# Kernel optimization log

Hardware: AMD Instinct MI355X
Metric: run time of the kernel (lower is better)

Reference implementation:

```python
import jax, jax.numpy as jnp
import numpy as np

N = 50000      # nodes
E = 800000     # edges (before self loops)
IN = 128       # in_channels
HID = 128      # 2*out_channels
OUT = 64       # out_channels
NEG_SLOPE = 0.2


def _gat_conv(x, src, dst, W, a_src, a_dst, b, n_nodes):
    """Single-head PyG GATConv (concat=True, heads=1, self-loops already added)."""
    h = x @ W                                   # [N, F]
    alpha_s = h @ a_src                         # [N]
    alpha_d = h @ a_dst                         # [N]
    e = alpha_s[src] + alpha_d[dst]             # [E'] logits per edge j->i
    e = jnp.where(e > 0, e, NEG_SLOPE * e)      # LeakyReLU(0.2)
    # segment softmax over destination node
    m = jax.ops.segment_max(e, dst, num_segments=n_nodes)   # [N]
    w = jnp.exp(e - m[dst])                                   # [E']
    denom = jax.ops.segment_sum(w, dst, num_segments=n_nodes) # [N]
    alpha = w / denom[dst]                                     # [E']
    out = jax.ops.segment_sum(alpha[:, None] * h[src], dst, num_segments=n_nodes)
    return out + b


def _with_self_loops(edge_index, n_nodes):
    loop = jnp.arange(n_nodes, dtype=edge_index.dtype)
    src = jnp.concatenate([edge_index[0], loop])
    dst = jnp.concatenate([edge_index[1], loop])
    return src, dst


def setup_inputs() -> dict:
    key = jax.random.key(0)
    ks = jax.random.split(key, 10)
    s = 0.1
    return {
        "x": jax.random.normal(ks[0], (N, IN), jnp.float32),
        "edge_index": jax.random.randint(ks[1], (2, E), 0, N, jnp.int32),
        "W1": jax.random.normal(ks[2], (IN, HID), jnp.float32) * s,
        "a1_src": jax.random.normal(ks[3], (HID,), jnp.float32) * s,
        "a1_dst": jax.random.normal(ks[4], (HID,), jnp.float32) * s,
        "b1": jnp.zeros((HID,), jnp.float32),
        "W2": jax.random.normal(ks[5], (HID, OUT), jnp.float32) * s,
        "a2_src": jax.random.normal(ks[6], (OUT,), jnp.float32) * s,
        "a2_dst": jax.random.normal(ks[7], (OUT,), jnp.float32) * s,
        "b2": jnp.zeros((OUT,), jnp.float32),
    }


def reference(x, edge_index, W1, a1_src, a1_dst, b1, W2, a2_src, a2_dst, b2):
    src, dst = _with_self_loops(edge_index, N)
    h = _gat_conv(x, src, dst, W1, a1_src, a1_dst, b1, N)
    h = jax.nn.relu(h)
    return _gat_conv(h, src, dst, W2, a2_src, a2_dst, b2, N)
```

## Files before the change

### kernel.cpp

```cpp
#include <hip/hip_runtime.h>
#include <hip/hip_bf16.h>


#define BCAP 4096

typedef __attribute__((ext_vector_type(8))) short bf16x8;
typedef __attribute__((ext_vector_type(4))) float f32x4;
typedef __attribute__((ext_vector_type(2))) float f32x2;

__device__ __forceinline__ unsigned short bf16bits(float f){
  __hip_bfloat16 b = __float2bfloat16(f);
  return *(unsigned short*)&b;
}
__device__ __forceinline__ float bf16lo(unsigned int v){ return __uint_as_float(v << 16); }
__device__ __forceinline__ float bf16hi(unsigned int v){ return __uint_as_float(v & 0xFFFF0000u); }
__device__ __forceinline__ f32x2 up2(unsigned int u){
  f32x2 r; r.x = __uint_as_float(u << 16); r.y = __uint_as_float(u & 0xFFFF0000u);
  return r;
}
__device__ __forceinline__ float leaky_exp(float e){
  e = (e > 0.f) ? e : 0.2f*e;
  return __expf(e);
}

__global__ __launch_bounds__(256) void prep_all(
    const float* __restrict__ W1, const float* __restrict__ W2,
    const float* __restrict__ a2s, const float* __restrict__ a2d,
    unsigned short* __restrict__ W1t, unsigned short* __restrict__ W2t,
    float* __restrict__ vas, float* __restrict__ vad,
    int* __restrict__ bucketCount)
{
  int b = blockIdx.x, t = threadIdx.x;
  if (b < 48){
    int idx = b*256 + t;
    if (idx < 8192){
      int n = idx >> 6, k2 = idx & 63;
      float a = W1[(size_t)(2*k2)*128 + n];
      float c = W1[(size_t)(2*k2+1)*128 + n];
      ushort2 o; o.x = bf16bits(a); o.y = bf16bits(c);
      *(ushort2*)&W1t[(size_t)n*128 + 2*k2] = o;
    } else {
      int r = idx - 8192;
      int n = r >> 6, k2 = r & 63;
      float a = W2[(size_t)(2*k2)*64 + n];
      float c = W2[(size_t)(2*k2+1)*64 + n];
      ushort2 o; o.x = bf16bits(a); o.y = bf16bits(c);
      *(ushort2*)&W2t[(size_t)n*128 + 2*k2] = o;
    }
  } else if (b == 48){
    int k = t & 127;
    const float* av = (t < 128) ? a2s : a2d;
    float* ov = (t < 128) ? vas : vad;
    float s = 0.f;
    for (int n=0; n<64; n++) s += W2[(size_t)k*64 + n] * av[n];
    ov[k] = s;
  } else {
    bucketCount[t] = 0; bucketCount[t+256] = 0;
  }
}

template<int NC, bool FUSE>
__device__ __forceinline__ void gemm_body(
    const float* __restrict__ Af, const unsigned short* __restrict__ Ah,
    const unsigned short* __restrict__ Wt,
    const float* __restrict__ avs, const float* __restrict__ avd,
    unsigned short* __restrict__ H, float* __restrict__ as_, float* __restrict__ ad_,
    int M, int rowBase, unsigned short* As, unsigned short* Ws)
{
  const int K = 128;
  int t = threadIdx.x;
  if (Af){
    #pragma unroll
    for (int i=0;i<8;i++){
      int idx = t + i*256; int r = idx>>5, k4 = idx&31;
      int grow = rowBase + r;
      float4 v = (grow<M) ? *(const float4*)&Af[(size_t)grow*K + k4*4]
                          : make_float4(0.f,0.f,0.f,0.f);
      ushort4 o; o.x=bf16bits(v.x); o.y=bf16bits(v.y); o.z=bf16bits(v.z); o.w=bf16bits(v.w);
      *(ushort4*)&As[r*136 + k4*4] = o;
    }
  } else {
    #pragma unroll
    for (int i=0;i<4;i++){
      int idx = t + i*256; int r = idx>>4, k8 = idx&15;
      int grow = rowBase + r;
      uint4 v = (grow<M) ? *(const uint4*)&Ah[(size_t)grow*K + k8*8]
                         : make_uint4(0u,0u,0u,0u);
      *(uint4*)&As[r*136 + k8*8] = v;
    }
  }
  int wave = t>>6, lane = t&63, ln = lane&15, q = lane>>4;
  f32x4 acc[NC/16];
  #pragma unroll
  for (int nt=0; nt<NC/16; nt++) acc[nt] = (f32x4){0.f,0.f,0.f,0.f};

  #pragma unroll
  for (int ch=0; ch<NC/64; ++ch){
    __syncthreads();
    #pragma unroll
    for (int i=0;i<4;i++){
      int idx = t + i*256; int n = idx>>4, k8 = idx&15;
      *(uint4*)&Ws[n*136 + k8*8] = *(const uint4*)&Wt[(size_t)(ch*64+n)*K + k8*8];
    }
    __syncthreads();
    #pragma unroll
    for (int kk=0;kk<4;kk++){
      bf16x8 a = *(const bf16x8*)&As[(wave*16+ln)*136 + kk*32 + q*8];
      #pragma unroll
      for (int nt=0; nt<4; nt++){
        bf16x8 b = *(const bf16x8*)&Ws[(nt*16+ln)*136 + kk*32 + q*8];
        acc[ch*4+nt] = __builtin_amdgcn_mfma_f32_16x16x32_bf16(a, b, acc[ch*4+nt], 0, 0, 0);
      }
    }
  }
  float asl[NC/16], adl[NC/16];
  if (FUSE){
    #pragma unroll
    for (int nt=0; nt<NC/16; nt++){ asl[nt]=avs[nt*16+ln]; adl[nt]=avd[nt*16+ln]; }
  }
  #pragma unroll
  for (int i=0;i<4;i++){
    int grow = rowBase + wave*16 + q*4 + i;
    if (grow < M){
      float ps=0.f, pd=0.f;
      #pragma unroll
      for (int nt=0; nt<NC/16; nt++){
        float v = acc[nt][i];
        H[(size_t)grow*NC + nt*16 + ln] = bf16bits(v);
        if (FUSE){ ps += v*asl[nt]; pd += v*adl[nt]; }
      }
      if (FUSE){
        #pragma unroll
        for (int d=1; d<16; d<<=1){ ps += __shfl_xor(ps,d); pd += __shfl_xor(pd,d); }
        if (ln==0){ as_[grow] = ps; ad_[grow] = pd; }
      }
    }
  }
}

__global__ __launch_bounds__(256) void scatter_or_gemm(
    const int* __restrict__ src, const int* __restrict__ dst,
    int* __restrict__ bucketCount, unsigned int* __restrict__ gbuf, int E, int SB,
    const float* __restrict__ x, const unsigned short* __restrict__ W1t,
    const float* __restrict__ a1s, const float* __restrict__ a1d,
    unsigned short* __restrict__ h1, float* __restrict__ as1, float* __restrict__ ad1,
    int M)
{
  __shared__ unsigned short smem[64*136 + 64*136];
  int t = threadIdx.x;
  if ((int)blockIdx.x >= SB){
    gemm_body<128, true>(x, nullptr, W1t, a1s, a1d, h1, as1, ad1, M,
                         (blockIdx.x - SB)*64, smem, smem + 64*136);
    return;
  }
  int* hist = (int*)smem;
  int* base = hist + 512;
  int e0 = blockIdx.x * 4096;
  hist[t] = 0; hist[t+256] = 0;
  __syncthreads();
  int sv[16], dv[16];
  #pragma unroll
  for (int k=0;k<16;k++){
    int i = e0 + t + k*256;
    if (i < E){ sv[k]=src[i]; dv[k]=dst[i]; atomicAdd(&hist[dv[k]>>7], 1); }
    else { sv[k] = -1; dv[k] = 0; }
  }
  __syncthreads();
  int h0 = hist[t], h1c = hist[t+256];
  if (h0 > 0)  base[t]     = atomicAdd(&bucketCount[t],     h0);
  if (h1c > 0) base[t+256] = atomicAdd(&bucketCount[t+256], h1c);
  __syncthreads();
  hist[t] = 0; hist[t+256] = 0;
  __syncthreads();
  #pragma unroll
  for (int k=0;k<16;k++){
    if (sv[k] >= 0){
      int b = dv[k] >> 7;
      int r = base[b] + atomicAdd(&hist[b], 1);
      if (r < BCAP)
        gbuf[(size_t)b*BCAP + r] = ((unsigned)(dv[k] & 127) << 16) | (unsigned)sv[k];
    }
  }
}

__global__ __launch_bounds__(512) void fine_sort(
    const unsigned int* __restrict__ gbuf, const int* __restrict__ bucketCount,
    int* __restrict__ offs, int* __restrict__ srcS,
    const float* __restrict__ as1, const float* __restrict__ ad1,
    float* __restrict__ wS1, unsigned short* __restrict__ dstS,
    int N, int E, int B)
{
  __shared__ int sh[512];
  __shared__ int h[128];
  __shared__ int pre[128];
  __shared__ int rank[128];
  int b = blockIdx.x, t = threadIdx.x;
  {
    int nd_t = 0;
    if (t < B){ int lo=t*128; nd_t = (N-lo<128)?(N-lo):128; }
    sh[t] = (t < B ? bucketCount[t] : 0) + nd_t;
    __syncthreads();
    for (int d=1; d<512; d<<=1){
      int x = (t >= d) ? sh[t-d] : 0;
      __syncthreads();
      sh[t] += x;
      __syncthreads();
    }
  }
  int cnt = bucketCount[b]; if (cnt > BCAP) cnt = BCAP;
  int lo = b*128;
  int nd = (N - lo < 128) ? (N - lo) : 128;
  int base = sh[b] - (cnt + nd);
  if (b == 0 && t == 0) offs[N] = E + N;
  if (t < 128){ h[t] = 0; rank[t] = 0; }
  __syncthreads();
  for (int i = t; i < cnt; i += 512)
    atomicAdd(&h[(gbuf[(size_t)b*BCAP + i] >> 16) & 127], 1);
  __syncthreads();
  if (t < 128) pre[t] = (t < nd) ? (h[t] + 1) : 0;
  __syncthreads();
  for (int d=1; d<128; d<<=1){
    int x = (t >= d && t < 128) ? pre[t-d] : 0;
    __syncthreads();
    if (t < 128) pre[t] += x;
    __syncthreads();
  }
  int seg = (t < nd) ? (h[t] + 1) : 0;
  int ex  = (t < 128) ? (pre[t] - seg) : 0;
  if (t < nd){
    int v = lo + t;
    offs[v] = base + ex;
    srcS[base + ex] = v;
    wS1[base + ex]  = leaky_exp(as1[v] + ad1[v]);
    dstS[base + ex] = (unsigned short)v;
  }
  __syncthreads();
  if (t < 128) pre[t] = ex;
  __syncthreads();
  for (int i = t; i < cnt; i += 512){
    unsigned e = gbuf[(size_t)b*BCAP + i];
    int dl = (e >> 16) & 127;
    int s  = e & 0xFFFF;
    int r  = atomicAdd(&rank[dl], 1);
    int pos = base + pre[dl] + 1 + r;
    srcS[pos] = s;
    wS1[pos]  = leaky_exp(as1[s] + ad1[lo + dl]);
    dstS[pos] = (unsigned short)(lo + dl);
  }
}

__global__ __launch_bounds__(256) void edge_agg128(
    const int* __restrict__ offs, const int* __restrict__ srcS,
    const float* __restrict__ wS,
    const unsigned short* __restrict__ Hin, const float* __restrict__ bias,
    unsigned short* __restrict__ outp,
    const float* __restrict__ vas, const float* __restrict__ vad,
    float* __restrict__ as2, float* __restrict__ ad2, int n)
{
  int wid  = (blockIdx.x * 256 + threadIdx.x) >> 6;
  int lane = threadIdx.x & 63;
  int qw = lane >> 4, ql = lane & 15;
  int v = wid*4 + qw;
  bool alive = (v < n);
  int beg = 0, end = 0;
  if (alive){ beg = offs[v]; end = offs[v+1]; }
  f32x2 acc2[4];
  #pragma unroll
  for (int c=0;c<4;c++) acc2[c] = (f32x2){0.f, 0.f};
  float dn = 0.f;
  for (int base = beg; base < end; base += 16){
    int m = end - base; if (m > 16) m = 16;
    int sv = 0; float wv = 0.f;
    if (ql < m){ sv = srcS[base + ql]; wv = wS[base + ql]; }
    for (int j = 0; j < m; j += 4){
      int l0 = (qw<<4) + j;
      int   s0 = __shfl(sv,l0),   s1 = __shfl(sv,l0+1);
      int   s2 = __shfl(sv,l0+2), s3 = __shfl(sv,l0+3);
      float w0 = __shfl(wv,l0),   w1 = __shfl(wv,l0+1);
      float w2 = __shfl(wv,l0+2), w3 = __shfl(wv,l0+3);
      uint4 ha = *(const uint4*)&Hin[(size_t)s0*128 + ql*8];
      uint4 hb = *(const uint4*)&Hin[(size_t)s1*128 + ql*8];
      uint4 hc = *(const uint4*)&Hin[(size_t)s2*128 + ql*8];
      uint4 hd = *(const uint4*)&Hin[(size_t)s3*128 + ql*8];
      dn += (w0 + w1) + (w2 + w3);
      acc2[0] += w0*up2(ha.x) + w1*up2(hb.x) + w2*up2(hc.x) + w3*up2(hd.x);
      acc2[1] += w0*up2(ha.y) + w1*up2(hb.y) + w2*up2(hc.y) + w3*up2(hd.y);
      acc2[2] += w0*up2(ha.z) + w1*up2(hb.z) + w2*up2(hc.z) + w3*up2(hd.z);
      acc2[3] += w0*up2(ha.w) + w1*up2(hb.w) + w2*up2(hc.w) + w3*up2(hd.w);
    }
  }
  if (alive){
    float accf[8];
    #pragma unroll
    for (int c=0;c<4;c++){ accf[2*c] = acc2[c].x; accf[2*c+1] = acc2[c].y; }
    float inv = 1.0f / dn;
    float ps = 0.f, pd = 0.f;
    unsigned short o[8];
    #pragma unroll
    for (int k=0;k<8;k++){
      float u = fmaxf(accf[k]*inv + bias[ql*8+k], 0.f);
      o[k] = bf16bits(u);
      ps += u * vas[ql*8+k];
      pd += u * vad[ql*8+k];
    }
    *(uint4*)&outp[(size_t)v*128 + ql*8] = *(uint4*)o;
    #pragma unroll
    for (int d2=1; d2<16; d2<<=1){ ps += __shfl_xor(ps,d2); pd += __shfl_xor(pd,d2); }
    if (ql == 0){ as2[v] = ps; ad2[v] = pd; }
  }
}

__global__ __launch_bounds__(256) void gemm2_or_wprep(
    const unsigned short* __restrict__ A, const unsigned short* __restrict__ Wt,
    unsigned short* __restrict__ H, int M, int G2B,
    const int* __restrict__ srcS, const unsigned short* __restrict__ dstS,
    const float* __restrict__ as2, const float* __restrict__ ad2,
    float* __restrict__ wS2, int T)
{
  __shared__ unsigned short smem[64*136 + 64*136];
  if ((int)blockIdx.x < G2B){
    gemm_body<64, false>(nullptr, A, Wt, nullptr, nullptr, H, nullptr, nullptr,
                         M, blockIdx.x*64, smem, smem + 64*136);
    return;
  }
  int i0 = (blockIdx.x - G2B)*256 + threadIdx.x;
  int stride = (gridDim.x - G2B)*256;
  for (int e = i0; e < T; e += stride){
    int s = srcS[e];
    int d = dstS[e];
    wS2[e] = leaky_exp(as2[s] + ad2[d]);
  }
}

__global__ __launch_bounds__(256) void edge_agg64(
    const int* __restrict__ offs, const int* __restrict__ srcS,
    const float* __restrict__ wS,
    const unsigned short* __restrict__ Hin, const float* __restrict__ bias,
    float* __restrict__ outp, int n)
{
  int wid  = (blockIdx.x * 256 + threadIdx.x) >> 6;
  int lane = threadIdx.x & 63;
  int ew = lane >> 3, el = lane & 7;
  int v = wid*8 + ew;
  bool alive = (v < n);
  int beg = 0, end = 0;
  if (alive){ beg = offs[v]; end = offs[v+1]; }
  f32x2 acc2[4];
  #pragma unroll
  for (int c=0;c<4;c++) acc2[c] = (f32x2){0.f, 0.f};
  float dn = 0.f;
  for (int base = beg; base < end; base += 8){
    int m = end - base; if (m > 8) m = 8;
    int sv = 0; float wv = 0.f;
    if (el < m){ sv = srcS[base + el]; wv = wS[base + el]; }
    for (int j = 0; j < m; j += 4){
      int l0 = (ew<<3) + j;
      int   s0 = __shfl(sv,l0),   s1 = __shfl(sv,l0+1);
      int   s2 = __shfl(sv,l0+2), s3 = __shfl(sv,l0+3);
      float w0 = __shfl(wv,l0),   w1 = __shfl(wv,l0+1);
      float w2 = __shfl(wv,l0+2), w3 = __shfl(wv,l0+3);
      uint4 ha = *(const uint4*)&Hin[(size_t)s0*64 + el*8];
      uint4 hb = *(const uint4*)&Hin[(size_t)s1*64 + el*8];
      uint4 hc = *(const uint4*)&Hin[(size_t)s2*64 + el*8];
      uint4 hd = *(const uint4*)&Hin[(size_t)s3*64 + el*8];
      dn += (w0 + w1) + (w2 + w3);
      acc2[0] += w0*up2(ha.x) + w1*up2(hb.x) + w2*up2(hc.x) + w3*up2(hd.x);
      acc2[1] += w0*up2(ha.y) + w1*up2(hb.y) + w2*up2(hc.y) + w3*up2(hd.y);
      acc2[2] += w0*up2(ha.z) + w1*up2(hb.z) + w2*up2(hc.z) + w3*up2(hd.z);
      acc2[3] += w0*up2(ha.w) + w1*up2(hb.w) + w2*up2(hc.w) + w3*up2(hd.w);
    }
  }
  if (alive){
    float inv = 1.0f / dn;
    float4 o0, o1;
    o0.x = acc2[0].x*inv + bias[el*8+0]; o0.y = acc2[0].y*inv + bias[el*8+1];
    o0.z = acc2[1].x*inv + bias[el*8+2]; o0.w = acc2[1].y*inv + bias[el*8+3];
    o1.x = acc2[2].x*inv + bias[el*8+4]; o1.y = acc2[2].y*inv + bias[el*8+5];
    o1.z = acc2[3].x*inv + bias[el*8+6]; o1.w = acc2[3].y*inv + bias[el*8+7];
    *(float4*)&outp[(size_t)v*64 + el*8]     = o0;
    *(float4*)&outp[(size_t)v*64 + el*8 + 4] = o1;
  }
}

extern "C" void kernel_launch(void* const* d_in, const int* in_sizes, int n_in,
                              void* d_out, int out_size, void* d_ws, size_t ws_size,
                              hipStream_t stream) {
  const int IN = 128, HID = 128, OUT = 64;
  const int N = in_sizes[0] / IN;
  const int E = in_sizes[1] / 2;
  const int B = (N + 127) / 128;
  const int SB = (E + 4095) / 4096;
  const int T = E + N;

  const float* x    = (const float*)d_in[0];
  const int*   ei   = (const int*)d_in[1];
  const float* W1   = (const float*)d_in[2];
  const float* a1s  = (const float*)d_in[3];
  const float* a1d  = (const float*)d_in[4];
  const float* b1   = (const float*)d_in[5];
  const float* W2   = (const float*)d_in[6];
  const float* a2s  = (const float*)d_in[7];
  const float* a2d  = (const float*)d_in[8];
  const float* b2   = (const float*)d_in[9];
  float* out = (float*)d_out;

  char* w = (char*)d_ws;
  unsigned short* W1t = (unsigned short*)w; w += (size_t)HID*IN*2;
  unsigned short* W2t = (unsigned short*)w; w += (size_t)OUT*HID*2;
  unsigned short* h1    = (unsigned short*)w; w += (size_t)N*128*2;
  unsigned short* hrelu = (unsigned short*)w; w += (size_t)N*128*2;
  unsigned short* h2 = h1;
  float* as1   = (float*)w; w += (size_t)N*4;
  float* ad1   = (float*)w; w += (size_t)N*4;
  float* as2   = (float*)w; w += (size_t)N*4;
  float* ad2   = (float*)w; w += (size_t)N*4;
  float* vas   = (float*)w; w += 128*4;
  float* vad   = (float*)w; w += 128*4;
  int* offs    = (int*)w;   w += (size_t)(N+1)*4;
  int* bucketCount = (int*)w; w += 512*4;
  int* srcS    = (int*)w;   w += (size_t)T*4;
  float* wS1   = (float*)w; w += (size_t)T*4;
  float* wS2   = (float*)w; w += (size_t)T*4;
  unsigned short* dstS = (unsigned short*)w; w += ((size_t)T*2 + 3) & ~(size_t)3;
  unsigned int* gbuf = (unsigned int*)w; w += (size_t)B*BCAP*4;

  const int* esrc = ei;
  const int* edst = ei + E;

  hipLaunchKernelGGL(prep_all, dim3(50), dim3(256), 0, stream,
                     W1, W2, a2s, a2d, W1t, W2t, vas, vad, bucketCount);
  hipLaunchKernelGGL(scatter_or_gemm, dim3(SB + (N+63)/64), dim3(256), 0, stream,
                     esrc, edst, bucketCount, gbuf, E, SB,
                     x, W1t, a1s, a1d, h1, as1, ad1, N);
  hipLaunchKernelGGL(fine_sort, dim3(B), dim3(512), 0, stream,
                     gbuf, bucketCount, offs, srcS, as1, ad1, wS1, dstS, N, E, B);
  int wv128 = (N + 3) / 4;
  hipLaunchKernelGGL(edge_agg128, dim3((wv128 + 3) / 4), dim3(256), 0, stream,
                     offs, srcS, wS1, h1, b1, hrelu, vas, vad, as2, ad2, N);
  const int G2B = (N + 63) / 64;
  hipLaunchKernelGGL(gemm2_or_wprep, dim3(G2B + 512), dim3(256), 0, stream,
                     hrelu, W2t, h2, N, G2B, srcS, dstS, as2, ad2, wS2, T);
  int wv64 = (N + 7) / 8;
  hipLaunchKernelGGL(edge_agg64, dim3((wv64 + 3) / 4), dim3(256), 0, stream,
                     offs, srcS, wS2, h2, b2, out, N);
}
```

Before: 179.8 us.

## Order nodes by degree to balance work in edge aggregation kernels

Builds a degree histogram during fine_sort, then adds a deg_scatter kernel that writes a permutation grouping nodes by in-degree (capped at 63). Both edge aggregation kernels now process nodes through this permutation, so the sub-wave groups sharing a wavefront see similar loop trip counts and diverge less. In exchange it adds a kernel launch, global atomics for the histogram and ranks, an extra indirection per node, and less locality in the offs reads and output writes.

After: 449.4 us. +150.0%, slower.

```diff
diff --git a/kernel.cpp b/kernel.cpp
--- a/kernel.cpp
+++ b/kernel.cpp
@@ -28,7 +28,8 @@
     const float* __restrict__ a2s, const float* __restrict__ a2d,
     unsigned short* __restrict__ W1t, unsigned short* __restrict__ W2t,
     float* __restrict__ vas, float* __restrict__ vad,
-    int* __restrict__ bucketCount)
+    int* __restrict__ bucketCount, int* __restrict__ degHist,
+    int* __restrict__ degRank)
 {
   int b = blockIdx.x, t = threadIdx.x;
   if (b < 48){
@@ -56,6 +57,7 @@
     ov[k] = s;
   } else {
     bucketCount[t] = 0; bucketCount[t+256] = 0;
+    if (t < 64){ degHist[t] = 0; degRank[t] = 0; }
   }
 }
 
@@ -188,7 +190,7 @@
     int* __restrict__ offs, int* __restrict__ srcS,
     const float* __restrict__ as1, const float* __restrict__ ad1,
     float* __restrict__ wS1, unsigned short* __restrict__ dstS,
-    int N, int E, int B)
+    int* __restrict__ degHist, int N, int E, int B)
 {
   __shared__ int sh[512];
   __shared__ int h[128];
@@ -233,6 +235,8 @@
     srcS[base + ex] = v;
     wS1[base + ex]  = leaky_exp(as1[v] + ad1[v]);
     dstS[base + ex] = (unsigned short)v;
+    int deg = h[t] + 1; if (deg > 63) deg = 63;
+    atomicAdd(&degHist[deg], 1);
   }
   __syncthreads();
   if (t < 128) pre[t] = ex;
@@ -249,9 +253,28 @@
   }
 }
 
+__global__ __launch_bounds__(256) void deg_scatter(
+    const int* __restrict__ offs, const int* __restrict__ degHist,
+    int* __restrict__ degRank, int* __restrict__ perm, int N)
+{
+  __shared__ int base[64];
+  int t = threadIdx.x;
+  if (t < 64){
+    int s = 0;
+    for (int j = 0; j < t; j++) s += degHist[j];
+    base[t] = s;
+  }
+  __syncthreads();
+  for (int v = blockIdx.x*256 + t; v < N; v += gridDim.x*256){
+    int deg = offs[v+1] - offs[v]; if (deg > 63) deg = 63;
+    int pos = base[deg] + atomicAdd(&degRank[deg], 1);
+    perm[pos] = v;
+  }
+}
+
 __global__ __launch_bounds__(256) void edge_agg128(
     const int* __restrict__ offs, const int* __restrict__ srcS,
-    const float* __restrict__ wS,
+    const float* __restrict__ wS, const int* __restrict__ perm,
     const unsigned short* __restrict__ Hin, const float* __restrict__ bias,
     unsigned short* __restrict__ outp,
     const float* __restrict__ vas, const float* __restrict__ vad,
@@ -260,10 +283,10 @@
   int wid  = (blockIdx.x * 256 + threadIdx.x) >> 6;
   int lane = threadIdx.x & 63;
   int qw = lane >> 4, ql = lane & 15;
-  int v = wid*4 + qw;
-  bool alive = (v < n);
-  int beg = 0, end = 0;
-  if (alive){ beg = offs[v]; end = offs[v+1]; }
+  int idx = wid*4 + qw;
+  bool alive = (idx < n);
+  int v = 0, beg = 0, end = 0;
+  if (alive){ v = perm[idx]; beg = offs[v]; end = offs[v+1]; }
   f32x2 acc2[4];
   #pragma unroll
   for (int c=0;c<4;c++) acc2[c] = (f32x2){0.f, 0.f};
@@ -334,17 +357,17 @@
 
 __global__ __launch_bounds__(256) void edge_agg64(
     const int* __restrict__ offs, const int* __restrict__ srcS,
-    const float* __restrict__ wS,
+    const float* __restrict__ wS, const int* __restrict__ perm,
     const unsigned short* __restrict__ Hin, const float* __restrict__ bias,
     float* __restrict__ outp, int n)
 {
   int wid  = (blockIdx.x * 256 + threadIdx.x) >> 6;
   int lane = threadIdx.x & 63;
   int ew = lane >> 3, el = lane & 7;
-  int v = wid*8 + ew;
-  bool alive = (v < n);
-  int beg = 0, end = 0;
-  if (alive){ beg = offs[v]; end = offs[v+1]; }
+  int idx = wid*8 + ew;
+  bool alive = (idx < n);
+  int v = 0, beg = 0, end = 0;
+  if (alive){ v = perm[idx]; beg = offs[v]; end = offs[v+1]; }
   f32x2 acc2[4];
   #pragma unroll
   for (int c=0;c<4;c++) acc2[c] = (f32x2){0.f, 0.f};
@@ -418,6 +441,9 @@
   float* vad   = (float*)w; w += 128*4;
   int* offs    = (int*)w;   w += (size_t)(N+1)*4;
   int* bucketCount = (int*)w; w += 512*4;
+  int* degHist = (int*)w;   w += 64*4;
+  int* degRank = (int*)w;   w += 64*4;
+  int* perm    = (int*)w;   w += (size_t)N*4;
   int* srcS    = (int*)w;   w += (size_t)T*4;
   float* wS1   = (float*)w; w += (size_t)T*4;
   float* wS2   = (float*)w; w += (size_t)T*4;
@@ -428,19 +454,23 @@
   const int* edst = ei + E;
 
   hipLaunchKernelGGL(prep_all, dim3(50), dim3(256), 0, stream,
-                     W1, W2, a2s, a2d, W1t, W2t, vas, vad, bucketCount);
+                     W1, W2, a2s, a2d, W1t, W2t, vas, vad, bucketCount,
+                     degHist, degRank);
   hipLaunchKernelGGL(scatter_or_gemm, dim3(SB + (N+63)/64), dim3(256), 0, stream,
                      esrc, edst, bucketCount, gbuf, E, SB,
                      x, W1t, a1s, a1d, h1, as1, ad1, N);
   hipLaunchKernelGGL(fine_sort, dim3(B), dim3(512), 0, stream,
-                     gbuf, bucketCount, offs, srcS, as1, ad1, wS1, dstS, N, E, B);
+                     gbuf, bucketCount, offs, srcS, as1, ad1, wS1, dstS,
+                     degHist, N, E, B);
+  hipLaunchKernelGGL(deg_scatter, dim3(128), dim3(256), 0, stream,
+                     offs, degHist, degRank, perm, N);
   int wv128 = (N + 3) / 4;
   hipLaunchKernelGGL(edge_agg128, dim3((wv128 + 3) / 4), dim3(256), 0, stream,
-                     offs, srcS, wS1, h1, b1, hrelu, vas, vad, as2, ad2, N);
+                     offs, srcS, wS1, perm, h1, b1, hrelu, vas, vad, as2, ad2, N);
   const int G2B = (N + 63) / 64;
   hipLaunchKernelGGL(gemm2_or_wprep, dim3(G2B + 512), dim3(256), 0, stream,
                      hrelu, W2t, h2, N, G2B, srcS, dstS, as2, ad2, wS2, T);
   int wv64 = (N + 7) / 8;
   hipLaunchKernelGGL(edge_agg64, dim3((wv64 + 3) / 4), dim3(256), 0, stream,
-                     offs, srcS, wS2, h2, b2, out, N);
-}
+                     offs, srcS, wS2, perm, h2, b2, out, N);
+}
```
